# Performance work log

Measured on AMD Instinct MI355X. Metric: run time of the kernel, lower is better.

## Reference

```python
import jax, jax.numpy as jnp
import numpy as np

D_MODEL = 256; N_HEADS = 8; N_LEVELS = 4; N_POINTS = 4; D_FFN = 1024
BS = 8; NQ = 100; NKPT = 17
LEVEL_SHAPES = [(160, 160), (80, 80), (40, 40), (20, 20)]  # (H, W) per level
LEN_V = sum(h * w for h, w in LEVEL_SHAPES)  # 34000


def layer_norm(x, g, b, eps=1e-5):
    m = x.mean(-1, keepdims=True)
    v = ((x - m) ** 2).mean(-1, keepdims=True)
    return (x - m) * jax.lax.rsqrt(v + eps) * g + b


def mha(q, k, v, Wqkv, bqkv, Wo, bo):
    # torch nn.MultiheadAttention, batch_first, eval mode (no dropout)
    d = q.shape[-1]; dh = d // N_HEADS
    def proj(x, W, b):
        return (x @ W.T + b).reshape(*x.shape[:-1], N_HEADS, dh)
    qp = proj(q, Wqkv[:d], bqkv[:d])
    kp = proj(k, Wqkv[d:2 * d], bqkv[d:2 * d])
    vp = proj(v, Wqkv[2 * d:], bqkv[2 * d:])
    att = jnp.einsum('bqhd,bkhd->bhqk', qp, kp) / jnp.sqrt(jnp.asarray(dh, q.dtype))
    att = jax.nn.softmax(att, -1)
    out = jnp.einsum('bhqk,bkhd->bqhd', att, vp).reshape(q.shape)
    return out @ Wo.T + bo


def bilinear_sample(val, loc, h, w):
    # val: (B, H, h*w, Dh); loc: (B, Lq, H, P, 2) normalized to [0,1]
    # matches F.grid_sample(align_corners=False, padding_mode='zeros') on grid 2*loc-1
    B, Lq, H, P, _ = loc.shape
    px = loc[..., 0] * w - 0.5
    py = loc[..., 1] * h - 0.5
    x0f = jnp.floor(px); y0f = jnp.floor(py)
    lx = px - x0f; ly = py - y0f
    x0 = x0f.astype(jnp.int32); y0 = y0f.astype(jnp.int32)
    out = jnp.zeros((B, H, Lq, P, val.shape[-1]), val.dtype)
    for dx, dy, wt in ((0, 0, (1 - lx) * (1 - ly)), (1, 0, lx * (1 - ly)),
                       (0, 1, (1 - lx) * ly), (1, 1, lx * ly)):
        xi = x0 + dx; yi = y0 + dy
        valid = ((xi >= 0) & (xi < w) & (yi >= 0) & (yi < h)).astype(val.dtype)
        idx = jnp.clip(yi, 0, h - 1) * w + jnp.clip(xi, 0, w - 1)  # (B,Lq,H,P)
        idx = idx.transpose(0, 2, 1, 3).reshape(B, H, Lq * P)
        g = jnp.take_along_axis(val, idx[..., None], axis=2).reshape(B, H, Lq, P, -1)
        out = out + g * (wt * valid).transpose(0, 2, 1, 3)[..., None]
    return out  # (B, H, Lq, P, Dh)


def ms_deform_attn(query, ref_points, memory, off_W, off_b, aw_W, aw_b,
                   val_W, val_b, outp_W, outp_b):
    B, Lq, _ = query.shape
    dh = D_MODEL // N_HEADS
    value = (memory @ val_W.T + val_b).reshape(B, LEN_V, N_HEADS, dh)
    off = (query @ off_W.T + off_b).reshape(B, Lq, N_HEADS, N_LEVELS, N_POINTS, 2)
    aw = (query @ aw_W.T + aw_b).reshape(B, Lq, N_HEADS, N_LEVELS * N_POINTS)
    aw = jax.nn.softmax(aw, -1).reshape(B, Lq, N_HEADS, N_LEVELS, N_POINTS)
    normalizer = jnp.array([[w, h] for h, w in LEVEL_SHAPES], dtype=query.dtype)  # (L,2) as (W,H)
    loc = ref_points[:, :, None, :, None, :] + off / normalizer[None, None, None, :, None, :]
    out = jnp.zeros((B, Lq, N_HEADS, dh), query.dtype)
    start = 0
    for l, (h, w) in enumerate(LEVEL_SHAPES):
        vl = value[:, start:start + h * w].transpose(0, 2, 1, 3)  # (B,H,hw,Dh)
        s = bilinear_sample(vl, loc[:, :, :, l], h, w)            # (B,H,Lq,P,Dh)
        out = out + jnp.einsum('bhqpd,bqhp->bqhd', s, aw[:, :, :, l])
        start += h * w
    return out.reshape(B, Lq, D_MODEL) @ outp_W.T + outp_b


def setup_inputs() -> dict:
    key = jax.random.key(0)
    ks = iter(jax.random.split(key, 40))
    d = D_MODEL
    def w(shape, s=0.02):
        return jax.random.normal(next(ks), shape, jnp.float32) * s
    inp = {
        'tgt_pose': jax.random.normal(next(ks), (BS, NQ, NKPT, d), jnp.float32),
        'tgt_pose_query_pos': jax.random.normal(next(ks), (BS, NQ, NKPT, d), jnp.float32),
        'tgt_pose_reference_points': jax.random.uniform(next(ks), (BS, NQ * NKPT, N_LEVELS, 2), jnp.float32),
        'memory': jax.random.normal(next(ks), (BS, LEN_V, d), jnp.float32),
        'win_Wqkv': w((3 * d, d)), 'win_bqkv': jnp.zeros((3 * d,), jnp.float32),
        'win_Wo': w((d, d)), 'win_bo': jnp.zeros((d,), jnp.float32),
        'win_ng': jnp.ones((d,), jnp.float32), 'win_nb': jnp.zeros((d,), jnp.float32),
        'acr_Wqkv': w((3 * d, d)), 'acr_bqkv': jnp.zeros((3 * d,), jnp.float32),
        'acr_Wo': w((d, d)), 'acr_bo': jnp.zeros((d,), jnp.float32),
        'acr_ng': jnp.ones((d,), jnp.float32), 'acr_nb': jnp.zeros((d,), jnp.float32),
        'off_W': w((N_HEADS * N_LEVELS * N_POINTS * 2, d)),
        'off_b': jax.random.uniform(next(ks), (N_HEADS * N_LEVELS * N_POINTS * 2,), jnp.float32, -1.0, 1.0),
        'aw_W': w((N_HEADS * N_LEVELS * N_POINTS, d)), 'aw_b': jnp.zeros((N_HEADS * N_LEVELS * N_POINTS,), jnp.float32),
        'val_W': w((d, d)), 'val_b': jnp.zeros((d,), jnp.float32),
        'outp_W': w((d, d)), 'outp_b': jnp.zeros((d,), jnp.float32),
        'gate_W': w((2 * d, 2 * d)), 'gate_b': jnp.zeros((2 * d,), jnp.float32),
        'gate_ng': jnp.ones((d,), jnp.float32), 'gate_nb': jnp.zeros((d,), jnp.float32),
        'ffn_W1': w((D_FFN, d)), 'ffn_b1': jnp.zeros((D_FFN,), jnp.float32),
        'ffn_W2': w((d, D_FFN)), 'ffn_b2': jnp.zeros((d,), jnp.float32),
        'n2_g': jnp.ones((d,), jnp.float32), 'n2_b': jnp.zeros((d,), jnp.float32),
        'memory_spatial_shapes': jnp.array(LEVEL_SHAPES, jnp.int32),
    }
    return inp


def reference(tgt_pose, tgt_pose_query_pos, tgt_pose_reference_points, memory,
              win_Wqkv, win_bqkv, win_Wo, win_bo, win_ng, win_nb,
              acr_Wqkv, acr_bqkv, acr_Wo, acr_bo, acr_ng, acr_nb,
              off_W, off_b, aw_W, aw_b, val_W, val_b, outp_W, outp_b,
              gate_W, gate_b, gate_ng, gate_nb,
              ffn_W1, ffn_b1, ffn_W2, ffn_b2, n2_g, n2_b,
              memory_spatial_shapes):
    bs, nq, K, d = tgt_pose.shape
    # with_pos_embed mutates tgt_pose in place in the torch code -> residual includes pos
    tgt = tgt_pose + tgt_pose_query_pos
    # within-attention over keypoints of each query
    x = tgt.reshape(bs * nq, K, d)
    t2 = mha(x, x, x, win_Wqkv, win_bqkv, win_Wo, win_bo).reshape(bs, nq, K, d)
    tgt = layer_norm(tgt + t2, win_ng, win_nb)
    # across-attention over queries for each keypoint
    xk = tgt.transpose(0, 2, 1, 3).reshape(bs * K, nq, d)
    t2 = mha(xk, xk, xk, acr_Wqkv, acr_bqkv, acr_Wo, acr_bo)
    tgt = layer_norm(xk + t2, acr_ng, acr_nb).reshape(bs, K, nq, d).transpose(0, 2, 1, 3)
    # second in-place pos add before deformable cross-attn (also feeds gateway)
    tgt_q = tgt + tgt_pose_query_pos
    t2 = ms_deform_attn(tgt_q.reshape(bs, nq * K, d), tgt_pose_reference_points, memory,
                        off_W, off_b, aw_W, aw_b, val_W, val_b, outp_W, outp_b)
    t2 = t2.reshape(bs, nq, K, d)
    # Gate
    g = jax.nn.sigmoid(jnp.concatenate([tgt_q, t2], -1) @ gate_W.T + gate_b)
    g1, g2 = jnp.split(g, 2, -1)
    tgt = layer_norm(g1 * tgt_q + g2 * t2, gate_ng, gate_nb)
    # FFN
    h = jax.nn.relu(tgt @ ffn_W1.T + ffn_b1)
    tgt = tgt + h @ ffn_W2.T + ffn_b2
    tgt = layer_norm(jnp.clip(tgt, -65504.0, 65504.0), n2_g, n2_b)
    return tgt
```

## Files before the change

kernel.cpp:

```cpp
#include <hip/hip_runtime.h>
#include <hip/hip_bf16.h>

#define NH 8
#define BS_ 8
#define NQ_ 100
#define NK_ 17
#define LQ 1700
#define T_TOK 13600
#define LEN_VV 34000

typedef __attribute__((ext_vector_type(8))) short short8v;
typedef __attribute__((ext_vector_type(8))) __bf16 bf16x8;
typedef __attribute__((ext_vector_type(4))) float f32x4;

__device__ __forceinline__ short f2bf(float f){
  __hip_bfloat16 h = __float2bfloat16(f);
  return *reinterpret_cast<short*>(&h);
}
__device__ __forceinline__ float bf2f(short s){
  return __uint_as_float(((uint)(unsigned short)s) << 16);
}

template<int EPI, int ADDA, int SWZ>
__global__ __launch_bounds__(256) void mgemm_k(const float* __restrict__ A,
                                               const float* __restrict__ A2,
                                               const float* __restrict__ W,
                                               const float* __restrict__ bias,
                                               __hip_bfloat16* __restrict__ Cb,
                                               int M, int N, int K, int nbx){
  __shared__ short sh[128 * 136];
  short* As = sh;
  short* Ws = sh + 128 * 64;
  int j;
  if (SWZ){
    int total = gridDim.x;
    int q = total >> 3, r = total & 7;
    int x = blockIdx.x & 7, k = blockIdx.x >> 3;
    j = (x < r) ? x * (q + 1) + k : r * (q + 1) + (x - r) * q + k;
  } else {
    j = blockIdx.x;
  }
  const int tid = threadIdx.x;
  const int bm = (j / nbx) * 128, bn = (j % nbx) * 128;
  const int wave = tid >> 6, lane = tid & 63;
  const int wm = (wave >> 1) * 64, wn = (wave & 1) * 64;
  const int s = tid & 7;
  const int row0 = tid >> 3;
  f32x4 acc[4][4] = {};
  const int lrow = lane & 15, lk = lane >> 4;

  float4 ra[8], rw[8];
#pragma unroll
  for (int i = 0; i < 4; i++){
    int row = row0 + i * 32;
    int gr = bm + row;
    float4 z = make_float4(0.f, 0.f, 0.f, 0.f);
    if (gr < M){
      const float* p = A + (size_t)gr * K + s * 8;
      float4 x0 = ((const float4*)p)[0], x1 = ((const float4*)p)[1];
      if (ADDA){
        const float* q2 = A2 + (size_t)gr * K + s * 8;
        float4 y0 = ((const float4*)q2)[0], y1 = ((const float4*)q2)[1];
        x0.x+=y0.x; x0.y+=y0.y; x0.z+=y0.z; x0.w+=y0.w;
        x1.x+=y1.x; x1.y+=y1.y; x1.z+=y1.z; x1.w+=y1.w;
      }
      ra[2 * i] = x0; ra[2 * i + 1] = x1;
    } else { ra[2 * i] = z; ra[2 * i + 1] = z; }
    const float* q = W + (size_t)(bn + row) * K + s * 8;
    rw[2 * i] = ((const float4*)q)[0]; rw[2 * i + 1] = ((const float4*)q)[1];
  }

  for (int k0 = 0; k0 < K; k0 += 64){
#pragma unroll
    for (int i = 0; i < 4; i++){
      int row = row0 + i * 32;
      int sw = ((s ^ (row & 7)) << 3) + row * 64;
      float4 a0 = ra[2 * i], a1 = ra[2 * i + 1];
      short8v v;
      v[0]=f2bf(a0.x); v[1]=f2bf(a0.y); v[2]=f2bf(a0.z); v[3]=f2bf(a0.w);
      v[4]=f2bf(a1.x); v[5]=f2bf(a1.y); v[6]=f2bf(a1.z); v[7]=f2bf(a1.w);
      *(short8v*)&As[sw] = v;
      a0 = rw[2 * i]; a1 = rw[2 * i + 1];
      short8v u;
      u[0]=f2bf(a0.x); u[1]=f2bf(a0.y); u[2]=f2bf(a0.z); u[3]=f2bf(a0.w);
      u[4]=f2bf(a1.x); u[5]=f2bf(a1.y); u[6]=f2bf(a1.z); u[7]=f2bf(a1.w);
      *(short8v*)&Ws[sw] = u;
    }
    __syncthreads();
    if (k0 + 64 < K){
#pragma unroll
      for (int i = 0; i < 4; i++){
        int row = row0 + i * 32;
        int gr = bm + row;
        float4 z = make_float4(0.f, 0.f, 0.f, 0.f);
        if (gr < M){
          const float* p = A + (size_t)gr * K + k0 + 64 + s * 8;
          float4 x0 = ((const float4*)p)[0], x1 = ((const float4*)p)[1];
          if (ADDA){
            const float* q2 = A2 + (size_t)gr * K + k0 + 64 + s * 8;
            float4 y0 = ((const float4*)q2)[0], y1 = ((const float4*)q2)[1];
            x0.x+=y0.x; x0.y+=y0.y; x0.z+=y0.z; x0.w+=y0.w;
            x1.x+=y1.x; x1.y+=y1.y; x1.z+=y1.z; x1.w+=y1.w;
          }
          ra[2 * i] = x0; ra[2 * i + 1] = x1;
        } else { ra[2 * i] = z; ra[2 * i + 1] = z; }
        const float* q = W + (size_t)(bn + row) * K + k0 + 64 + s * 8;
        rw[2 * i] = ((const float4*)q)[0]; rw[2 * i + 1] = ((const float4*)q)[1];
      }
    }
#pragma unroll
    for (int ks = 0; ks < 2; ks++){
      short8v af[4], bw[4];
      int slot = ks * 4 + lk;
#pragma unroll
      for (int m = 0; m < 4; m++){
        int r = wm + m * 16 + lrow;
        af[m] = *(const short8v*)&As[r * 64 + ((slot ^ (r & 7)) << 3)];
      }
#pragma unroll
      for (int n = 0; n < 4; n++){
        int r = wn + n * 16 + lrow;
        bw[n] = *(const short8v*)&Ws[r * 64 + ((slot ^ (r & 7)) << 3)];
      }
#pragma unroll
      for (int m = 0; m < 4; m++)
#pragma unroll
        for (int n = 0; n < 4; n++)
          acc[m][n] = __builtin_amdgcn_mfma_f32_16x16x32_bf16(
              __builtin_bit_cast(bf16x8, af[m]),
              __builtin_bit_cast(bf16x8, bw[n]), acc[m][n], 0, 0, 0);
    }
    __syncthreads();
  }
  const int STR = 136;
#pragma unroll
  for (int n = 0; n < 4; n++){
    int col = wn + n * 16 + lrow;
    float bsv = bias[bn + col];
#pragma unroll
    for (int m = 0; m < 4; m++){
#pragma unroll
      for (int i = 0; i < 4; i++){
        int row = wm + m * 16 + lk * 4 + i;
        float c = acc[m][n][i] + bsv;
        if (EPI == 1) c = fmaxf(c, 0.f);
        sh[row * STR + col] = f2bf(c);
      }
    }
  }
  __syncthreads();
#pragma unroll
  for (int it = 0; it < 8; it++){
    int r = it * 16 + (tid >> 4);
    int chunk = tid & 15;
    if (bm + r < M){
      uint4 v = *(const uint4*)((const char*)sh + r * 272 + chunk * 16);
      *(uint4*)((char*)Cb + ((size_t)(bm + r) * N + bn) * 2 + chunk * 16) = v;
    }
  }
}

template<int EPI, int OUTB, int INB, int DUALA>
__global__ __launch_bounds__(256) void g64_k(const void* __restrict__ Av,
                                             const void* __restrict__ A1v,
                                             const float* __restrict__ W0,
                                             const float* __restrict__ W1,
                                             int NSPLIT,
                                             const float* __restrict__ bias0,
                                             const float* __restrict__ bias1,
                                             const float* __restrict__ RES,
                                             float* __restrict__ Cf,
                                             __hip_bfloat16* __restrict__ Cb,
                                             int M, int N, int K, int sA){
  __shared__ short sh64[2 * 64 * 64];
  short* As = sh64;
  short* Ws = sh64 + 64 * 64;
  const int tid = threadIdx.x;
  const int bn = blockIdx.x * 64, bm = blockIdx.y * 64;
  const int wave = tid >> 6, lane = tid & 63;
  const int wm = (wave >> 1) * 32, wn = (wave & 1) * 32;
  const int s = tid & 7, row0 = tid >> 3;
  const int lrow = lane & 15, lk = lane >> 4;
  f32x4 acc[2][2] = {};

  for (int k0 = 0; k0 < K; k0 += 64){
#pragma unroll
    for (int i = 0; i < 2; i++){
      int row = row0 + i * 32;
      int sw = ((s ^ (row & 7)) << 3) + row * 64;
      short8v v = {};
      int gr = bm + row;
      if (gr < M){
        if (INB){
          v = *(const short8v*)((const short*)Av + (size_t)gr * sA + k0 + s * 8);
        } else {
          const float* Ap;
          if (DUALA) Ap = (k0 < 256) ? (const float*)Av + (size_t)gr * 256 + k0
                                     : (const float*)A1v + (size_t)gr * 256 + (k0 - 256);
          else Ap = (const float*)Av + (size_t)gr * sA + k0;
          float4 a0 = ((const float4*)(Ap + s * 8))[0];
          float4 a1 = ((const float4*)(Ap + s * 8))[1];
          v[0]=f2bf(a0.x); v[1]=f2bf(a0.y); v[2]=f2bf(a0.z); v[3]=f2bf(a0.w);
          v[4]=f2bf(a1.x); v[5]=f2bf(a1.y); v[6]=f2bf(a1.z); v[7]=f2bf(a1.w);
        }
      }
      *(short8v*)&As[sw] = v;
      int wr = bn + row;
      const float* Wp = (wr < NSPLIT) ? W0 + (size_t)wr * K + k0
                                      : W1 + (size_t)(wr - NSPLIT) * K + k0;
      float4 b0 = ((const float4*)(Wp + s * 8))[0];
      float4 b1 = ((const float4*)(Wp + s * 8))[1];
      short8v u;
      u[0]=f2bf(b0.x); u[1]=f2bf(b0.y); u[2]=f2bf(b0.z); u[3]=f2bf(b0.w);
      u[4]=f2bf(b1.x); u[5]=f2bf(b1.y); u[6]=f2bf(b1.z); u[7]=f2bf(b1.w);
      *(short8v*)&Ws[sw] = u;
    }
    __syncthreads();
#pragma unroll
    for (int ks = 0; ks < 2; ks++){
      int slot = ks * 4 + lk;
      short8v af[2], bw[2];
#pragma unroll
      for (int m = 0; m < 2; m++){
        int r = wm + m * 16 + lrow;
        af[m] = *(const short8v*)&As[r * 64 + ((slot ^ (r & 7)) << 3)];
      }
#pragma unroll
      for (int n = 0; n < 2; n++){
        int r = wn + n * 16 + lrow;
        bw[n] = *(const short8v*)&Ws[r * 64 + ((slot ^ (r & 7)) << 3)];
      }
#pragma unroll
      for (int m = 0; m < 2; m++)
#pragma unroll
        for (int n = 0; n < 2; n++)
          acc[m][n] = __builtin_amdgcn_mfma_f32_16x16x32_bf16(
              __builtin_bit_cast(bf16x8, af[m]),
              __builtin_bit_cast(bf16x8, bw[n]), acc[m][n], 0, 0, 0);
    }
    __syncthreads();
  }
  if (OUTB){
    const int STR = 72;
#pragma unroll
    for (int n = 0; n < 2; n++){
      int col = wn + n * 16 + lrow;
      int gc = bn + col;
      float bsv = (gc < NSPLIT) ? bias0[gc] : bias1[gc - NSPLIT];
#pragma unroll
      for (int m = 0; m < 2; m++){
#pragma unroll
        for (int i = 0; i < 4; i++){
          int row = wm + m * 16 + lk * 4 + i;
          float c = acc[m][n][i] + bsv;
          if (EPI == 1) c = fmaxf(c, 0.f);
          if (EPI == 2) c = 1.f / (1.f + expf(-c));
          sh64[row * STR + col] = f2bf(c);
        }
      }
    }
    __syncthreads();
#pragma unroll
    for (int it = 0; it < 2; it++){
      int r = it * 32 + (tid >> 3);
      int chunk = tid & 7;
      if (bm + r < M){
        uint4 v = *(const uint4*)((const char*)sh64 + r * 144 + chunk * 16);
        *(uint4*)((char*)Cb + ((size_t)(bm + r) * N + bn) * 2 + chunk * 16) = v;
      }
    }
  } else {
#pragma unroll
    for (int n = 0; n < 2; n++){
      int gc = bn + wn + n * 16 + lrow;
      float bsv = (gc < NSPLIT) ? bias0[gc] : bias1[gc - NSPLIT];
#pragma unroll
      for (int m = 0; m < 2; m++){
#pragma unroll
        for (int i = 0; i < 4; i++){
          int row = bm + wm + m * 16 + lk * 4 + i;
          if (row >= M) continue;
          float c = acc[m][n][i] + bsv;
          if (EPI == 1) c = fmaxf(c, 0.f);
          if (EPI == 2) c = 1.f / (1.f + expf(-c));
          if (EPI == 3) c += RES[(size_t)row * N + gc];
          Cf[(size_t)row * N + gc] = c;
        }
      }
    }
  }
}

template<int SITE, int OUTB>
__global__ __launch_bounds__(512) void gln_k(const short* __restrict__ Abf,
                                             const float* __restrict__ W,
                                             const float* __restrict__ bias,
                                             const float* __restrict__ r0,
                                             const float* __restrict__ r1,
                                             const float* __restrict__ g,
                                             const float* __restrict__ be,
                                             void* __restrict__ outv,
                                             int M, int K){
  __shared__ short As[64 * 64];
  __shared__ short Ws[256 * 64];
  __shared__ float part[64][4][2];
  __shared__ float stats[64][2];
  const int tid = threadIdx.x;
  const int bm = blockIdx.x * 64;
  const int wave = tid >> 6, lane = tid & 63;
  const int wm = (wave >> 2) * 32, wn = (wave & 3) * 64;
  const int s = tid & 7, row0 = tid >> 3;
  const int lrow = lane & 15, lk = lane >> 4;
  f32x4 acc[2][4] = {};

  short8v pa = {};
  { int gr = bm + row0; if (gr < M) pa = *(const short8v*)(Abf + (size_t)gr * K + s * 8); }
  float4 pw[8];
#pragma unroll
  for (int i = 0; i < 4; i++){
    const float* wp = W + (size_t)(row0 + i * 64) * K + s * 8;
    pw[2 * i] = ((const float4*)wp)[0]; pw[2 * i + 1] = ((const float4*)wp)[1];
  }

  for (int k0 = 0; k0 < K; k0 += 64){
    *(short8v*)&As[row0 * 64 + ((s ^ (row0 & 7)) << 3)] = pa;
#pragma unroll
    for (int i = 0; i < 4; i++){
      int row = row0 + i * 64;
      float4 b0 = pw[2 * i], b1 = pw[2 * i + 1];
      short8v u;
      u[0]=f2bf(b0.x); u[1]=f2bf(b0.y); u[2]=f2bf(b0.z); u[3]=f2bf(b0.w);
      u[4]=f2bf(b1.x); u[5]=f2bf(b1.y); u[6]=f2bf(b1.z); u[7]=f2bf(b1.w);
      *(short8v*)&Ws[row * 64 + ((s ^ (row & 7)) << 3)] = u;
    }
    __syncthreads();
    if (k0 + 64 < K){
      int gr = bm + row0;
      pa = (short8v){};
      if (gr < M) pa = *(const short8v*)(Abf + (size_t)gr * K + k0 + 64 + s * 8);
#pragma unroll
      for (int i = 0; i < 4; i++){
        const float* wp = W + (size_t)(row0 + i * 64) * K + k0 + 64 + s * 8;
        pw[2 * i] = ((const float4*)wp)[0]; pw[2 * i + 1] = ((const float4*)wp)[1];
      }
    }
#pragma unroll
    for (int ks = 0; ks < 2; ks++){
      int slot = ks * 4 + lk;
      short8v af[2], bw[4];
#pragma unroll
      for (int m = 0; m < 2; m++){
        int r = wm + m * 16 + lrow;
        af[m] = *(const short8v*)&As[r * 64 + ((slot ^ (r & 7)) << 3)];
      }
#pragma unroll
      for (int n = 0; n < 4; n++){
        int r = wn + n * 16 + lrow;
        bw[n] = *(const short8v*)&Ws[r * 64 + ((slot ^ (r & 7)) << 3)];
      }
#pragma unroll
      for (int m = 0; m < 2; m++)
#pragma unroll
        for (int n = 0; n < 4; n++)
          acc[m][n] = __builtin_amdgcn_mfma_f32_16x16x32_bf16(
              __builtin_bit_cast(bf16x8, af[m]),
              __builtin_bit_cast(bf16x8, bw[n]), acc[m][n], 0, 0, 0);
    }
    __syncthreads();
  }

#pragma unroll
  for (int m = 0; m < 2; m++){
#pragma unroll
    for (int i = 0; i < 4; i++){
      int row = wm + m * 16 + lk * 4 + i;
      int grow = bm + row;
      float s1 = 0.f, s2 = 0.f;
      if (grow < M){
#pragma unroll
        for (int n = 0; n < 4; n++){
          int col = wn + n * 16 + lrow;
          float x = acc[m][n][i] + bias[col] + r0[(size_t)grow * 256 + col];
          if (SITE == 0) x += r1[(size_t)grow * 256 + col];
          if (SITE == 2) x = fminf(fmaxf(x, -65504.f), 65504.f);
          acc[m][n][i] = x;
          s1 += x; s2 += x * x;
        }
      }
#pragma unroll
      for (int msk = 1; msk <= 8; msk <<= 1){
        s1 += __shfl_xor(s1, msk, 64);
        s2 += __shfl_xor(s2, msk, 64);
      }
      if (lrow == 0){ part[row][wave & 3][0] = s1; part[row][wave & 3][1] = s2; }
    }
  }
  __syncthreads();
  if (tid < 64){
    float s1 = part[tid][0][0] + part[tid][1][0] + part[tid][2][0] + part[tid][3][0];
    float s2 = part[tid][0][1] + part[tid][1][1] + part[tid][2][1] + part[tid][3][1];
    float mean = s1 * (1.f / 256.f);
    float var = s2 * (1.f / 256.f) - mean * mean;
    stats[tid][0] = mean;
    stats[tid][1] = rsqrtf(fmaxf(var, 0.f) + 1e-5f);
  }
  __syncthreads();
#pragma unroll
  for (int m = 0; m < 2; m++){
#pragma unroll
    for (int i = 0; i < 4; i++){
      int row = wm + m * 16 + lk * 4 + i;
      int grow = bm + row;
      if (grow >= M) continue;
      float mean = stats[row][0], rstd = stats[row][1];
      size_t orow = grow;
      if (SITE == 0){
        int bi = grow / LQ; int rem = grow % LQ; int q = rem / NK_; int kk = rem % NK_;
        orow = (size_t)bi * LQ + kk * NQ_ + q;
      }
      if (SITE == 1){
        int bi = grow / LQ; int rem = grow % LQ; int kk = rem / NQ_; int q = rem % NQ_;
        orow = (size_t)bi * LQ + q * NK_ + kk;
      }
#pragma unroll
      for (int n = 0; n < 4; n++){
        int col = wn + n * 16 + lrow;
        float o = (acc[m][n][i] - mean) * rstd * g[col] + be[col];
        if (SITE == 1) o += r1[orow * 256 + col];
        if (OUTB) ((short*)outv)[orow * 256 + col] = f2bf(o);
        else      ((float*)outv)[orow * 256 + col] = o;
      }
    }
  }
}

__global__ __launch_bounds__(512) void gateln_k(const short* __restrict__ TQ,
                                                const short* __restrict__ T2,
                                                const float* __restrict__ W,
                                                const float* __restrict__ bias,
                                                const float* __restrict__ g,
                                                const float* __restrict__ be,
                                                float* __restrict__ out, int M){
  __shared__ short sh[64 * 64 + 512 * 64];
  short* As = sh;
  short* Ws = sh + 64 * 64;
  const int tid = threadIdx.x;
  const int bm = blockIdx.x * 64;
  const int wave = tid >> 6, lane = tid & 63;
  const int wm = (wave >> 2) * 32, wn = (wave & 3) * 128;
  const int s = tid & 7, row0 = tid >> 3;
  const int lrow = lane & 15, lk = lane >> 4;
  f32x4 acc[2][8] = {};

  for (int k0 = 0; k0 < 512; k0 += 64){
    {
      short8v v = {};
      int gr = bm + row0;
      if (gr < M){
        v = (k0 < 256) ? *(const short8v*)(TQ + (size_t)gr * 256 + k0 + s * 8)
                       : *(const short8v*)(T2 + (size_t)gr * 256 + (k0 - 256) + s * 8);
      }
      *(short8v*)&As[row0 * 64 + ((s ^ (row0 & 7)) << 3)] = v;
    }
#pragma unroll
    for (int i = 0; i < 8; i++){
      int row = row0 + i * 64;
      const float* wp = W + (size_t)row * 512 + k0 + s * 8;
      float4 b0 = ((const float4*)wp)[0], b1 = ((const float4*)wp)[1];
      short8v u;
      u[0]=f2bf(b0.x); u[1]=f2bf(b0.y); u[2]=f2bf(b0.z); u[3]=f2bf(b0.w);
      u[4]=f2bf(b1.x); u[5]=f2bf(b1.y); u[6]=f2bf(b1.z); u[7]=f2bf(b1.w);
      *(short8v*)&Ws[row * 64 + ((s ^ (row & 7)) << 3)] = u;
    }
    __syncthreads();
#pragma unroll
    for (int ks = 0; ks < 2; ks++){
      int slot = ks * 4 + lk;
      short8v af[2], bw[8];
#pragma unroll
      for (int m = 0; m < 2; m++){
        int r = wm + m * 16 + lrow;
        af[m] = *(const short8v*)&As[r * 64 + ((slot ^ (r & 7)) << 3)];
      }
#pragma unroll
      for (int n = 0; n < 8; n++){
        int r = wn + n * 16 + lrow;
        bw[n] = *(const short8v*)&Ws[r * 64 + ((slot ^ (r & 7)) << 3)];
      }
#pragma unroll
      for (int m = 0; m < 2; m++)
#pragma unroll
        for (int n = 0; n < 8; n++)
          acc[m][n] = __builtin_amdgcn_mfma_f32_16x16x32_bf16(
              __builtin_bit_cast(bf16x8, af[m]),
              __builtin_bit_cast(bf16x8, bw[n]), acc[m][n], 0, 0, 0);
    }
    __syncthreads();
  }
  short* gb = sh;
  const int GSTR = 520;
#pragma unroll
  for (int n = 0; n < 8; n++){
    int col = wn + n * 16 + lrow;
    float bsv = bias[col];
#pragma unroll
    for (int m = 0; m < 2; m++){
#pragma unroll
      for (int i = 0; i < 4; i++){
        int row = wm + m * 16 + lk * 4 + i;
        float c = acc[m][n][i] + bsv;
        gb[row * GSTR + col] = f2bf(1.f / (1.f + __expf(-c)));
      }
    }
  }
  __syncthreads();
  {
    int row = tid >> 3, cg = tid & 7;
    int grow = bm + row;
    float x[32];
    float s1 = 0.f, s2 = 0.f;
    if (grow < M){
#pragma unroll
      for (int jv = 0; jv < 4; jv++){
        int c0 = cg * 32 + jv * 8;
        short8v aqv = *(const short8v*)(TQ + (size_t)grow * 256 + c0);
        short8v t2v = *(const short8v*)(T2 + (size_t)grow * 256 + c0);
#pragma unroll
        for (int jj = 0; jj < 8; jj++){
          float g1 = bf2f(gb[row * GSTR + c0 + jj]);
          float g2 = bf2f(gb[row * GSTR + 256 + c0 + jj]);
          float xv = g1 * bf2f(aqv[jj]) + g2 * bf2f(t2v[jj]);
          x[jv * 8 + jj] = xv; s1 += xv; s2 += xv * xv;
        }
      }
    }
    s1 += __shfl_xor(s1, 1, 64); s2 += __shfl_xor(s2, 1, 64);
    s1 += __shfl_xor(s1, 2, 64); s2 += __shfl_xor(s2, 2, 64);
    s1 += __shfl_xor(s1, 4, 64); s2 += __shfl_xor(s2, 4, 64);
    float mean = s1 * (1.f / 256.f);
    float var = s2 * (1.f / 256.f) - mean * mean;
    float rstd = rsqrtf(fmaxf(var, 0.f) + 1e-5f);
    if (grow < M){
#pragma unroll
      for (int jv = 0; jv < 4; jv++){
        int c0 = cg * 32 + jv * 8;
        float4 o0, o1;
        float* po = (float*)&o0;
#pragma unroll
        for (int jj = 0; jj < 8; jj++){
          int c = c0 + jj;
          float o = (x[jv * 8 + jj] - mean) * rstd * g[c] + be[c];
          if (jj < 4) ((float*)&o0)[jj] = o; else ((float*)&o1)[jj - 4] = o;
        }
        (void)po;
        *(float4*)(out + (size_t)grow * 256 + c0) = o0;
        *(float4*)(out + (size_t)grow * 256 + c0 + 4) = o1;
      }
    }
  }
}

template<int TP, int NSPL>
__global__ __launch_bounds__(256) void mha_mfma_k(const short* __restrict__ qkv,
                                                  __hip_bfloat16* __restrict__ out, int S){
  constexpr int MT = TP / 16;
  constexpr int KSTEPS = (TP + 31) / 32;
  constexpr int KS32 = KSTEPS * 32;
  constexpr int VSTRB = (KS32 == 128) ? 256 : 128;
  constexpr int CH = (MT + NSPL - 1) / NSPL;
  __shared__ short QK[2][TP][64];
  __shared__ short Vt[2][32][VSTRB / 2];
  __shared__ float Sc[2][16][128];
  __shared__ float rinv[2][16];

  const int tid = threadIdx.x;
  const int bid = blockIdx.x;
  const int batch = bid / (4 * NSPL);
  const int rem = bid % (4 * NSPL);
  const int hp = rem / NSPL;
  const int half = rem % NSPL;
  const int mtlo = half * CH;
  const int mthi = (mtlo + CH < MT) ? (mtlo + CH) : MT;
  const int wave = tid >> 6, lane = tid & 63;
  const int hh = wave >> 1, wsub = wave & 1;
  const int lrow = lane & 15, lk = lane >> 4;
  const float scale = 0.17677669529663687f;
  const size_t qbase = (size_t)batch * S * 768;

  for (int idx = tid; idx < 2 * TP * 4; idx += 256){
    int h2 = idx >= TP * 4;
    int rm = idx - h2 * TP * 4;
    int j = rm >> 2, s = rm & 3;
    int h = hp * 2 + h2;
    short8v qv = {}, kv = {};
    if (j < S){
      const short* p = qkv + qbase + (size_t)j * 768 + h * 32 + s * 8;
      qv = *(const short8v*)p;
      kv = *(const short8v*)(p + 256);
    }
    *(short8v*)&QK[h2][j][(s ^ (j & 7)) << 3] = qv;
    *(short8v*)&QK[h2][j][((s + 4) ^ (j & 7)) << 3] = kv;
  }
  for (int idx = tid; idx < 2 * KS32 * 4; idx += 256){
    int h2 = idx >= KS32 * 4;
    int rm = idx - h2 * KS32 * 4;
    int j = rm >> 2, e8 = rm & 3;
    int h = hp * 2 + h2;
    short8v v = {};
    if (j < S) v = *(const short8v*)(qkv + qbase + (size_t)j * 768 + h * 32 + 512 + e8 * 8);
#pragma unroll
    for (int c = 0; c < 8; c++){
      int e = e8 * 8 + c;
      char* pb = (char*)&Vt[h2][0][0] + e * VSTRB + (((j >> 3) ^ (e & 7)) << 4) + ((j & 7) << 1);
      *(short*)pb = v[c];
    }
  }
  __syncthreads();

  for (int mt = mtlo; mt < mthi; mt++){
    for (int nt = wsub; nt < MT; nt += 2){
      int ar = mt * 16 + lrow;
      short8v aq = *(const short8v*)&QK[hh][ar][(lk ^ (ar & 7)) << 3];
      int br = nt * 16 + lrow;
      short8v bk = *(const short8v*)&QK[hh][br][((lk + 4) ^ (br & 7)) << 3];
      f32x4 z = {};
      f32x4 d = __builtin_amdgcn_mfma_f32_16x16x32_bf16(
          __builtin_bit_cast(bf16x8, aq), __builtin_bit_cast(bf16x8, bk), z, 0, 0, 0);
#pragma unroll
      for (int i = 0; i < 4; i++){
        int rr = lk * 4 + i;
        int c = nt * 16 + lrow;
        Sc[hh][rr][(((c >> 2) ^ (rr & 7)) << 2) + (c & 3)] = d[i] * scale;
      }
    }
    __syncthreads();
    if (wsub == 0){
      int rr = lane >> 2, p = lane & 3;
      int grow = mt * 16 + rr;
      int Seff = (grow < S) ? S : 0;
      float mx = -1e30f;
#pragma unroll
      for (int m = 0; m < KSTEPS; m++){
        int j = p + 4 * m;
#pragma unroll
        for (int hf = 0; hf < 2; hf++){
          int ls = 2 * j + hf;
          float4 v = *(const float4*)&Sc[hh][rr][(ls ^ (rr & 7)) << 2];
          int c0 = ls * 4;
          mx = fmaxf(mx, (c0 + 0 < Seff) ? v.x : -1e30f);
          mx = fmaxf(mx, (c0 + 1 < Seff) ? v.y : -1e30f);
          mx = fmaxf(mx, (c0 + 2 < Seff) ? v.z : -1e30f);
          mx = fmaxf(mx, (c0 + 3 < Seff) ? v.w : -1e30f);
        }
      }
      mx = fmaxf(mx, __shfl_xor(mx, 1, 64));
      mx = fmaxf(mx, __shfl_xor(mx, 2, 64));
      float sum = 0.f;
#pragma unroll
      for (int m = 0; m < KSTEPS; m++){
        int j = p + 4 * m;
        float ev[8];
#pragma unroll
        for (int hf = 0; hf < 2; hf++){
          int ls = 2 * j + hf;
          float4 v = *(const float4*)&Sc[hh][rr][(ls ^ (rr & 7)) << 2];
          int c0 = ls * 4;
          ev[hf * 4 + 0] = (c0 + 0 < Seff) ? __expf(v.x - mx) : 0.f;
          ev[hf * 4 + 1] = (c0 + 1 < Seff) ? __expf(v.y - mx) : 0.f;
          ev[hf * 4 + 2] = (c0 + 2 < Seff) ? __expf(v.z - mx) : 0.f;
          ev[hf * 4 + 3] = (c0 + 3 < Seff) ? __expf(v.w - mx) : 0.f;
        }
        short8v pb;
#pragma unroll
        for (int q2 = 0; q2 < 8; q2++){ pb[q2] = f2bf(ev[q2]); sum += ev[q2]; }
        *(short8v*)((char*)&Sc[hh][rr][0] + ((j ^ (rr & 7)) << 4)) = pb;
      }
      sum += __shfl_xor(sum, 1, 64);
      sum += __shfl_xor(sum, 2, 64);
      if (p == 0) rinv[hh][rr] = (sum > 0.f) ? 1.f / sum : 0.f;
    }
    __syncthreads();
    {
      int nt2 = wsub;
      f32x4 acc = {};
#pragma unroll
      for (int ks = 0; ks < KSTEPS; ks++){
        int slot = ks * 4 + lk;
        short8v ap = *(const short8v*)((const char*)&Sc[hh][lrow][0] + ((slot ^ (lrow & 7)) << 4));
        int e = nt2 * 16 + lrow;
        short8v bv = *(const short8v*)((const char*)&Vt[hh][0][0] + e * VSTRB + ((slot ^ (e & 7)) << 4));
        acc = __builtin_amdgcn_mfma_f32_16x16x32_bf16(
            __builtin_bit_cast(bf16x8, ap), __builtin_bit_cast(bf16x8, bv), acc, 0, 0, 0);
      }
      int h = hp * 2 + hh;
#pragma unroll
      for (int i = 0; i < 4; i++){
        int row = mt * 16 + lk * 4 + i;
        if (row < S){
          float rv = rinv[hh][lk * 4 + i];
          out[((size_t)batch * S + row) * 256 + h * 32 + nt2 * 16 + lrow] =
              __float2bfloat16(acc[i] * rv);
        }
      }
    }
    __syncthreads();
  }
}

__global__ __launch_bounds__(256) void deform_k(const __hip_bfloat16* __restrict__ val,
                                                const float* __restrict__ offaw,
                                                const float* __restrict__ ref,
                                                unsigned int* __restrict__ outb){
  __shared__ uint2 meta[32][16][4];
  const int tid = threadIdx.x;
  const int t0 = blockIdx.x * 4;
  {
    int g = tid >> 3;
    int pair = tid & 7;
    int lt = g >> 3, h = g & 7;
    int t = t0 + lt;
    int b = t / LQ;
    int p0 = pair * 2;
    int l = p0 >> 2;
    const int starts[4] = {0, 25600, 32000, 33600};
    const int HS[4] = {160, 80, 40, 20};
    int w = HS[l];
    const float* ap = offaw + (size_t)t * 384 + 256 + h * 16;
    float a0 = ap[p0];
    float a1 = ap[p0 + 1];
    float mx = fmaxf(a0, a1);
#pragma unroll
    for (int m = 1; m <= 4; m <<= 1) mx = fmaxf(mx, __shfl_xor(mx, m, 64));
    float e0 = expf(a0 - mx), e1 = expf(a1 - mx);
    float s = e0 + e1;
#pragma unroll
    for (int m = 1; m <= 4; m <<= 1) s += __shfl_xor(s, m, 64);
    float inv = 1.f / s;
    float rx = ref[((size_t)t * 4 + l) * 2 + 0];
    float ry = ref[((size_t)t * 4 + l) * 2 + 1];
    float4 ov = *(const float4*)(offaw + (size_t)t * 384 + h * 32 + l * 8 + p0 * 2);
    int vbase = (b * LEN_VV + starts[l]) * 128 + h * 16;
#pragma unroll
    for (int pp = 0; pp < 2; pp++){
      float wgt = (pp ? e1 : e0) * inv;
      float px = rx * w + (pp ? ov.z : ov.x) - 0.5f;
      float py = ry * w + (pp ? ov.w : ov.y) - 0.5f;
      float x0f = floorf(px), y0f = floorf(py);
      float lx = px - x0f, ly = py - y0f;
      int x0 = (int)x0f, y0 = (int)y0f;
#pragma unroll
      for (int c = 0; c < 4; c++){
        int dx = c & 1, dy = c >> 1;
        int xi = x0 + dx, yi = y0 + dy;
        bool ok = (xi >= 0) & (xi < w) & (yi >= 0) & (yi < w);
        float cw = ok ? wgt * (dx ? lx : 1.f - lx) * (dy ? ly : 1.f - ly) : 0.f;
        uint idx = ok ? (uint)(vbase + (yi * w + xi) * 128) : 0u;
        uint2 m2; m2.x = idx; m2.y = __float_as_uint(cw);
        meta[g][p0 + pp][c] = m2;
      }
    }
  }
  __syncthreads();
  const uint2* V2 = (const uint2*)val;
  int sg = tid >> 3, lane8 = tid & 7;
  int lt = sg >> 3, h = sg & 7;
  int t = t0 + lt;
  float a0 = 0.f, a1 = 0.f, a2 = 0.f, a3 = 0.f;
#pragma unroll 4
  for (int c = 0; c < 64; c++){
    uint2 mw = meta[sg][c >> 2][c & 3];
    float wv = __uint_as_float(mw.y);
    uint2 v = V2[(size_t)(mw.x >> 1) + lane8];
    a0 += wv * __uint_as_float(v.x << 16);
    a1 += wv * __uint_as_float(v.x & 0xffff0000u);
    a2 += wv * __uint_as_float(v.y << 16);
    a3 += wv * __uint_as_float(v.y & 0xffff0000u);
  }
  uint2 u;
  u.x = ((uint)(unsigned short)f2bf(a1) << 16) | (uint)(unsigned short)f2bf(a0);
  u.y = ((uint)(unsigned short)f2bf(a3) << 16) | (uint)(unsigned short)f2bf(a2);
  ((uint2*)outb)[((size_t)t * 256 + h * 32) / 4 + lane8] = u;
}

extern "C" void kernel_launch(void* const* d_in, const int* in_sizes, int n_in,
                              void* d_out, int out_size, void* d_ws, size_t ws_size,
                              hipStream_t stream){
  const float* tgt_pose = (const float*)d_in[0];
  const float* qpos     = (const float*)d_in[1];
  const float* refp     = (const float*)d_in[2];
  const float* memory   = (const float*)d_in[3];
  const float* win_Wqkv = (const float*)d_in[4];
  const float* win_bqkv = (const float*)d_in[5];
  const float* win_Wo   = (const float*)d_in[6];
  const float* win_bo   = (const float*)d_in[7];
  const float* win_ng   = (const float*)d_in[8];
  const float* win_nb   = (const float*)d_in[9];
  const float* acr_Wqkv = (const float*)d_in[10];
  const float* acr_bqkv = (const float*)d_in[11];
  const float* acr_Wo   = (const float*)d_in[12];
  const float* acr_bo   = (const float*)d_in[13];
  const float* acr_ng   = (const float*)d_in[14];
  const float* acr_nb   = (const float*)d_in[15];
  const float* off_W    = (const float*)d_in[16];
  const float* off_b    = (const float*)d_in[17];
  const float* aw_W     = (const float*)d_in[18];
  const float* aw_b     = (const float*)d_in[19];
  const float* val_W    = (const float*)d_in[20];
  const float* val_b    = (const float*)d_in[21];
  const float* outp_W   = (const float*)d_in[22];
  const float* outp_b   = (const float*)d_in[23];
  const float* gate_W   = (const float*)d_in[24];
  const float* gate_b   = (const float*)d_in[25];
  const float* gate_ng  = (const float*)d_in[26];
  const float* gate_nb  = (const float*)d_in[27];
  const float* ffn_W1   = (const float*)d_in[28];
  const float* ffn_b1   = (const float*)d_in[29];
  const float* ffn_W2   = (const float*)d_in[30];
  const float* ffn_b2   = (const float*)d_in[31];
  const float* n2_g     = (const float*)d_in[32];
  const float* n2_b     = (const float*)d_in[33];

  float* out = (float*)d_out;
  char* ws = (char*)d_ws;
  const size_t TB = (size_t)T_TOK * 256 * 4;
  float* B1 = (float*)(ws);
  float* B2 = (float*)(ws + TB);
  char* p = ws + 2 * TB;
  short* Qb  = (short*)p;  p += (size_t)T_TOK * 768 * 2;
  short* ABF = (short*)p;  p += (size_t)T_TOK * 256 * 2;
  short* TQb = (short*)p;  p += (size_t)T_TOK * 256 * 2;
  short* T2b = (short*)p;  p += (size_t)T_TOK * 256 * 2;
  float* OFFAW = (float*)p; p += (size_t)T_TOK * 384 * 4;
  char* Vregion = p;
  __hip_bfloat16* V = (__hip_bfloat16*)Vregion;
  short* FF = (short*)Vregion;

  const int GM128 = (T_TOK + 127) / 128;
  const int GM64  = (T_TOK + 63) / 64;
  const int BIG = 1 << 30;

  mgemm_k<0,0,1><<<2 * 2125, 256, 0, stream>>>(memory, nullptr, val_W, val_b, V, BS_ * LEN_VV, 256, 256, 2);
  mgemm_k<0,1,0><<<6 * GM128, 256, 0, stream>>>(tgt_pose, qpos, win_Wqkv, win_bqkv, (__hip_bfloat16*)Qb, T_TOK, 768, 256, 6);
  mha_mfma_k<32,1><<<800 * 4, 256, 0, stream>>>(Qb, (__hip_bfloat16*)ABF, 17);
  gln_k<0,0><<<GM64, 512, 0, stream>>>(ABF, win_Wo, win_bo, tgt_pose, qpos, win_ng, win_nb, B1, T_TOK, 256);
  mgemm_k<0,0,0><<<6 * GM128, 256, 0, stream>>>(B1, nullptr, acr_Wqkv, acr_bqkv, (__hip_bfloat16*)Qb, T_TOK, 768, 256, 6);
  mha_mfma_k<112,2><<<136 * 8, 256, 0, stream>>>(Qb, (__hip_bfloat16*)ABF, 100);
  gln_k<1,1><<<GM64, 512, 0, stream>>>(ABF, acr_Wo, acr_bo, B1, qpos, acr_ng, acr_nb, TQb, T_TOK, 256);
  g64_k<0,0,1,0><<<dim3(6, GM64), 256, 0, stream>>>(TQb, nullptr, off_W, aw_W, 256, off_b, aw_b, nullptr, OFFAW, nullptr, T_TOK, 384, 256, 256);
  deform_k<<<T_TOK / 4, 256, 0, stream>>>(V, OFFAW, refp, (unsigned int*)ABF);
  g64_k<0,1,1,0><<<dim3(4, GM64), 256, 0, stream>>>(ABF, nullptr, outp_W, outp_W, BIG, outp_b, outp_b, nullptr, nullptr, (__hip_bfloat16*)T2b, T_TOK, 256, 256, 256);
  gateln_k<<<GM64, 512, 0, stream>>>(TQb, T2b, gate_W, gate_b, gate_ng, gate_nb, B2, T_TOK);
  mgemm_k<1,0,0><<<8 * GM128, 256, 0, stream>>>(B2, nullptr, ffn_W1, ffn_b1, (__hip_bfloat16*)FF, T_TOK, 1024, 256, 8);
  gln_k<2,0><<<GM64, 512, 0, stream>>>(FF, ffn_W2, ffn_b2, B2, nullptr, n2_g, n2_b, out, T_TOK, 1024);
}
```

Measured before the change: 462.3 us.

## Fuse across-attn out-proj LayerNorm with offset/weight GEMM; store intermediate in bf16

Adds a kernel that computes the across-attention output projection, residual add and LayerNorm, adds the query position, and then runs the sampling-offset and attention-weight GEMM on the normalized tile held in shared memory. This removes one kernel launch and the global round trip of the TQ activations before the offset GEMM. The within-attention LayerNorm output is now stored as bf16 instead of fp32, and the QKV GEMM gains a bf16-input path, which halves that buffer's traffic and skips a conversion. In exchange the fused kernel has one block per 64 rows and reloads all 384 weight rows with a synchronisation at each K step, with no prefetch, so it may lose some parallelism and overlap.

```diff
diff --git a/kernel.cpp b/kernel.cpp
--- a/kernel.cpp
+++ b/kernel.cpp
@@ -21,8 +21,8 @@
   return __uint_as_float(((uint)(unsigned short)s) << 16);
 }
 
-template<int EPI, int ADDA, int SWZ>
-__global__ __launch_bounds__(256) void mgemm_k(const float* __restrict__ A,
+template<int EPI, int ADDA, int SWZ, int INB>
+__global__ __launch_bounds__(256) void mgemm_k(const void* __restrict__ Av,
                                                const float* __restrict__ A2,
                                                const float* __restrict__ W,
                                                const float* __restrict__ bias,
@@ -40,6 +40,8 @@
   } else {
     j = blockIdx.x;
   }
+  const float* A = (const float*)Av;
+  const short* Ab = (const short*)Av;
   const int tid = threadIdx.x;
   const int bm = (j / nbx) * 128, bn = (j % nbx) * 128;
   const int wave = tid >> 6, lane = tid & 63;
@@ -49,23 +51,29 @@
   f32x4 acc[4][4] = {};
   const int lrow = lane & 15, lk = lane >> 4;
 
-  float4 ra[8], rw[8];
+  float4 ra[INB ? 1 : 8], rw[8];
+  short8v rab[INB ? 4 : 1];
 #pragma unroll
   for (int i = 0; i < 4; i++){
     int row = row0 + i * 32;
     int gr = bm + row;
-    float4 z = make_float4(0.f, 0.f, 0.f, 0.f);
-    if (gr < M){
-      const float* p = A + (size_t)gr * K + s * 8;
-      float4 x0 = ((const float4*)p)[0], x1 = ((const float4*)p)[1];
-      if (ADDA){
-        const float* q2 = A2 + (size_t)gr * K + s * 8;
-        float4 y0 = ((const float4*)q2)[0], y1 = ((const float4*)q2)[1];
-        x0.x+=y0.x; x0.y+=y0.y; x0.z+=y0.z; x0.w+=y0.w;
-        x1.x+=y1.x; x1.y+=y1.y; x1.z+=y1.z; x1.w+=y1.w;
-      }
-      ra[2 * i] = x0; ra[2 * i + 1] = x1;
-    } else { ra[2 * i] = z; ra[2 * i + 1] = z; }
+    if (INB){
+      short8v z = {};
+      rab[INB ? i : 0] = (gr < M) ? *(const short8v*)(Ab + (size_t)gr * K + s * 8) : z;
+    } else {
+      float4 z = make_float4(0.f, 0.f, 0.f, 0.f);
+      if (gr < M){
+        const float* p = A + (size_t)gr * K + s * 8;
+        float4 x0 = ((const float4*)p)[0], x1 = ((const float4*)p)[1];
+        if (ADDA){
+          const float* q2 = A2 + (size_t)gr * K + s * 8;
+          float4 y0 = ((const float4*)q2)[0], y1 = ((const float4*)q2)[1];
+          x0.x+=y0.x; x0.y+=y0.y; x0.z+=y0.z; x0.w+=y0.w;
+          x1.x+=y1.x; x1.y+=y1.y; x1.z+=y1.z; x1.w+=y1.w;
+        }
+        ra[INB ? 0 : (2 * i)] = x0; ra[INB ? 0 : (2 * i + 1)] = x1;
+      } else { ra[INB ? 0 : (2 * i)] = z; ra[INB ? 0 : (2 * i + 1)] = z; }
+    }
     const float* q = W + (size_t)(bn + row) * K + s * 8;
     rw[2 * i] = ((const float4*)q)[0]; rw[2 * i + 1] = ((const float4*)q)[1];
   }
@@ -75,12 +83,16 @@
     for (int i = 0; i < 4; i++){
       int row = row0 + i * 32;
       int sw = ((s ^ (row & 7)) << 3) + row * 64;
-      float4 a0 = ra[2 * i], a1 = ra[2 * i + 1];
-      short8v v;
-      v[0]=f2bf(a0.x); v[1]=f2bf(a0.y); v[2]=f2bf(a0.z); v[3]=f2bf(a0.w);
-      v[4]=f2bf(a1.x); v[5]=f2bf(a1.y); v[6]=f2bf(a1.z); v[7]=f2bf(a1.w);
-      *(short8v*)&As[sw] = v;
-      a0 = rw[2 * i]; a1 = rw[2 * i + 1];
+      if (INB){
+        *(short8v*)&As[sw] = rab[INB ? i : 0];
+      } else {
+        float4 a0 = ra[INB ? 0 : (2 * i)], a1 = ra[INB ? 0 : (2 * i + 1)];
+        short8v v;
+        v[0]=f2bf(a0.x); v[1]=f2bf(a0.y); v[2]=f2bf(a0.z); v[3]=f2bf(a0.w);
+        v[4]=f2bf(a1.x); v[5]=f2bf(a1.y); v[6]=f2bf(a1.z); v[7]=f2bf(a1.w);
+        *(short8v*)&As[sw] = v;
+      }
+      float4 a0 = rw[2 * i], a1 = rw[2 * i + 1];
       short8v u;
       u[0]=f2bf(a0.x); u[1]=f2bf(a0.y); u[2]=f2bf(a0.z); u[3]=f2bf(a0.w);
       u[4]=f2bf(a1.x); u[5]=f2bf(a1.y); u[6]=f2bf(a1.z); u[7]=f2bf(a1.w);
@@ -92,18 +104,23 @@
       for (int i = 0; i < 4; i++){
         int row = row0 + i * 32;
         int gr = bm + row;
-        float4 z = make_float4(0.f, 0.f, 0.f, 0.f);
-        if (gr < M){
-          const float* p = A + (size_t)gr * K + k0 + 64 + s * 8;
-          float4 x0 = ((const float4*)p)[0], x1 = ((const float4*)p)[1];
-          if (ADDA){
-            const float* q2 = A2 + (size_t)gr * K + k0 + 64 + s * 8;
-            float4 y0 = ((const float4*)q2)[0], y1 = ((const float4*)q2)[1];
-            x0.x+=y0.x; x0.y+=y0.y; x0.z+=y0.z; x0.w+=y0.w;
-            x1.x+=y1.x; x1.y+=y1.y; x1.z+=y1.z; x1.w+=y1.w;
-          }
-          ra[2 * i] = x0; ra[2 * i + 1] = x1;
-        } else { ra[2 * i] = z; ra[2 * i + 1] = z; }
+        if (INB){
+          short8v z = {};
+          rab[INB ? i : 0] = (gr < M) ? *(const short8v*)(Ab + (size_t)gr * K + k0 + 64 + s * 8) : z;
+        } else {
+          float4 z = make_float4(0.f, 0.f, 0.f, 0.f);
+          if (gr < M){
+            const float* p = A + (size_t)gr * K + k0 + 64 + s * 8;
+            float4 x0 = ((const float4*)p)[0], x1 = ((const float4*)p)[1];
+            if (ADDA){
+              const float* q2 = A2 + (size_t)gr * K + k0 + 64 + s * 8;
+              float4 y0 = ((const float4*)q2)[0], y1 = ((const float4*)q2)[1];
+              x0.x+=y0.x; x0.y+=y0.y; x0.z+=y0.z; x0.w+=y0.w;
+              x1.x+=y1.x; x1.y+=y1.y; x1.z+=y1.z; x1.w+=y1.w;
+            }
+            ra[INB ? 0 : (2 * i)] = x0; ra[INB ? 0 : (2 * i + 1)] = x1;
+          } else { ra[INB ? 0 : (2 * i)] = z; ra[INB ? 0 : (2 * i + 1)] = z; }
+        }
         const float* q = W + (size_t)(bn + row) * K + k0 + 64 + s * 8;
         rw[2 * i] = ((const float4*)q)[0]; rw[2 * i + 1] = ((const float4*)q)[1];
       }
@@ -418,17 +435,216 @@
         int bi = grow / LQ; int rem = grow % LQ; int q = rem / NK_; int kk = rem % NK_;
         orow = (size_t)bi * LQ + kk * NQ_ + q;
       }
-      if (SITE == 1){
-        int bi = grow / LQ; int rem = grow % LQ; int kk = rem / NQ_; int q = rem % NQ_;
-        orow = (size_t)bi * LQ + q * NK_ + kk;
-      }
 #pragma unroll
       for (int n = 0; n < 4; n++){
         int col = wn + n * 16 + lrow;
         float o = (acc[m][n][i] - mean) * rstd * g[col] + be[col];
-        if (SITE == 1) o += r1[orow * 256 + col];
         if (OUTB) ((short*)outv)[orow * 256 + col] = f2bf(o);
         else      ((float*)outv)[orow * 256 + col] = o;
+      }
+    }
+  }
+}
+
+__global__ __launch_bounds__(512) void glnoa_k(const short* __restrict__ Abf,
+                                               const float* __restrict__ W,
+                                               const float* __restrict__ bias,
+                                               const short* __restrict__ r0b,
+                                               const float* __restrict__ qpos,
+                                               const float* __restrict__ g,
+                                               const float* __restrict__ be,
+                                               short* __restrict__ TQout,
+                                               float* __restrict__ OFFAW,
+                                               const float* __restrict__ off_W,
+                                               const float* __restrict__ aw_W,
+                                               const float* __restrict__ off_b,
+                                               const float* __restrict__ aw_b,
+                                               int M){
+  __shared__ short smem[64 * 256 + 384 * 64];
+  short* As1 = smem;
+  short* Ws1 = smem + 64 * 64;
+  float* part = (float*)(smem + 64 * 64 + 256 * 64);
+  float* stats = part + 64 * 4 * 2;
+  short* As2 = smem;
+  short* Ws2 = smem + 64 * 256;
+  const int K = 256;
+  const int tid = threadIdx.x;
+  const int bm = blockIdx.x * 64;
+  const int wave = tid >> 6, lane = tid & 63;
+  const int wm = (wave >> 2) * 32, wn = (wave & 3) * 64;
+  const int s = tid & 7, row0 = tid >> 3;
+  const int lrow = lane & 15, lk = lane >> 4;
+  f32x4 acc[2][4] = {};
+
+  short8v pa = {};
+  { int gr = bm + row0; if (gr < M) pa = *(const short8v*)(Abf + (size_t)gr * K + s * 8); }
+  float4 pw[8];
+#pragma unroll
+  for (int i = 0; i < 4; i++){
+    const float* wp = W + (size_t)(row0 + i * 64) * K + s * 8;
+    pw[2 * i] = ((const float4*)wp)[0]; pw[2 * i + 1] = ((const float4*)wp)[1];
+  }
+  for (int k0 = 0; k0 < K; k0 += 64){
+    *(short8v*)&As1[row0 * 64 + ((s ^ (row0 & 7)) << 3)] = pa;
+#pragma unroll
+    for (int i = 0; i < 4; i++){
+      int row = row0 + i * 64;
+      float4 b0 = pw[2 * i], b1 = pw[2 * i + 1];
+      short8v u;
+      u[0]=f2bf(b0.x); u[1]=f2bf(b0.y); u[2]=f2bf(b0.z); u[3]=f2bf(b0.w);
+      u[4]=f2bf(b1.x); u[5]=f2bf(b1.y); u[6]=f2bf(b1.z); u[7]=f2bf(b1.w);
+      *(short8v*)&Ws1[row * 64 + ((s ^ (row & 7)) << 3)] = u;
+    }
+    __syncthreads();
+    if (k0 + 64 < K){
+      int gr = bm + row0;
+      pa = (short8v){};
+      if (gr < M) pa = *(const short8v*)(Abf + (size_t)gr * K + k0 + 64 + s * 8);
+#pragma unroll
+      for (int i = 0; i < 4; i++){
+        const float* wp = W + (size_t)(row0 + i * 64) * K + k0 + 64 + s * 8;
+        pw[2 * i] = ((const float4*)wp)[0]; pw[2 * i + 1] = ((const float4*)wp)[1];
+      }
+    }
+#pragma unroll
+    for (int ks = 0; ks < 2; ks++){
+      int slot = ks * 4 + lk;
+      short8v af[2], bw[4];
+#pragma unroll
+      for (int m = 0; m < 2; m++){
+        int r = wm + m * 16 + lrow;
+        af[m] = *(const short8v*)&As1[r * 64 + ((slot ^ (r & 7)) << 3)];
+      }
+#pragma unroll
+      for (int n = 0; n < 4; n++){
+        int r = wn + n * 16 + lrow;
+        bw[n] = *(const short8v*)&Ws1[r * 64 + ((slot ^ (r & 7)) << 3)];
+      }
+#pragma unroll
+      for (int m = 0; m < 2; m++)
+#pragma unroll
+        for (int n = 0; n < 4; n++)
+          acc[m][n] = __builtin_amdgcn_mfma_f32_16x16x32_bf16(
+              __builtin_bit_cast(bf16x8, af[m]),
+              __builtin_bit_cast(bf16x8, bw[n]), acc[m][n], 0, 0, 0);
+    }
+    __syncthreads();
+  }
+#pragma unroll
+  for (int m = 0; m < 2; m++){
+#pragma unroll
+    for (int i = 0; i < 4; i++){
+      int row = wm + m * 16 + lk * 4 + i;
+      int grow = bm + row;
+      float s1 = 0.f, s2 = 0.f;
+      if (grow < M){
+#pragma unroll
+        for (int n = 0; n < 4; n++){
+          int col = wn + n * 16 + lrow;
+          float x = acc[m][n][i] + bias[col] + bf2f(r0b[(size_t)grow * 256 + col]);
+          acc[m][n][i] = x;
+          s1 += x; s2 += x * x;
+        }
+      }
+#pragma unroll
+      for (int msk = 1; msk <= 8; msk <<= 1){
+        s1 += __shfl_xor(s1, msk, 64);
+        s2 += __shfl_xor(s2, msk, 64);
+      }
+      if (lrow == 0){ part[(row * 4 + (wave & 3)) * 2] = s1; part[(row * 4 + (wave & 3)) * 2 + 1] = s2; }
+    }
+  }
+  __syncthreads();
+  if (tid < 64){
+    float s1 = part[(tid * 4 + 0) * 2] + part[(tid * 4 + 1) * 2] + part[(tid * 4 + 2) * 2] + part[(tid * 4 + 3) * 2];
+    float s2 = part[(tid * 4 + 0) * 2 + 1] + part[(tid * 4 + 1) * 2 + 1] + part[(tid * 4 + 2) * 2 + 1] + part[(tid * 4 + 3) * 2 + 1];
+    float mean = s1 * (1.f / 256.f);
+    float var = s2 * (1.f / 256.f) - mean * mean;
+    stats[tid * 2] = mean;
+    stats[tid * 2 + 1] = rsqrtf(fmaxf(var, 0.f) + 1e-5f);
+  }
+  __syncthreads();
+#pragma unroll
+  for (int m = 0; m < 2; m++){
+#pragma unroll
+    for (int i = 0; i < 4; i++){
+      int row = wm + m * 16 + lk * 4 + i;
+      int grow = bm + row;
+      float mean = stats[row * 2], rstd = stats[row * 2 + 1];
+      size_t orow = 0;
+      if (grow < M){
+        int bi = grow / LQ; int rem = grow % LQ; int kk = rem / NQ_; int q = rem % NQ_;
+        orow = (size_t)bi * LQ + q * NK_ + kk;
+      }
+#pragma unroll
+      for (int n = 0; n < 4; n++){
+        int col = wn + n * 16 + lrow;
+        float tq = 0.f;
+        if (grow < M){
+          float o = (acc[m][n][i] - mean) * rstd * g[col] + be[col];
+          tq = o + qpos[orow * 256 + col];
+          TQout[orow * 256 + col] = f2bf(tq);
+        }
+        As2[row * 256 + ((((col >> 3) ^ (row & 7)) << 3) + (col & 7))] = f2bf(tq);
+      }
+    }
+  }
+  __syncthreads();
+  const int wm2 = (wave >> 2) * 32, wn2 = (wave & 3) * 96;
+  f32x4 acc2[2][6] = {};
+  for (int k0 = 0; k0 < 256; k0 += 64){
+#pragma unroll
+    for (int it = 0; it < 6; it++){
+      int wr = row0 + it * 64;
+      const float* Wp = (wr < 256) ? off_W + (size_t)wr * 256 + k0
+                                   : aw_W + (size_t)(wr - 256) * 256 + k0;
+      float4 b0 = ((const float4*)(Wp + s * 8))[0];
+      float4 b1 = ((const float4*)(Wp + s * 8))[1];
+      short8v u;
+      u[0]=f2bf(b0.x); u[1]=f2bf(b0.y); u[2]=f2bf(b0.z); u[3]=f2bf(b0.w);
+      u[4]=f2bf(b1.x); u[5]=f2bf(b1.y); u[6]=f2bf(b1.z); u[7]=f2bf(b1.w);
+      *(short8v*)&Ws2[wr * 64 + ((s ^ (wr & 7)) << 3)] = u;
+    }
+    __syncthreads();
+#pragma unroll
+    for (int ks = 0; ks < 2; ks++){
+      int slotl = ks * 4 + lk;
+      int slotg = (k0 >> 3) + slotl;
+      short8v af[2], bw[6];
+#pragma unroll
+      for (int m = 0; m < 2; m++){
+        int r = wm2 + m * 16 + lrow;
+        af[m] = *(const short8v*)&As2[r * 256 + ((slotg ^ (r & 7)) << 3)];
+      }
+#pragma unroll
+      for (int n = 0; n < 6; n++){
+        int r = wn2 + n * 16 + lrow;
+        bw[n] = *(const short8v*)&Ws2[r * 64 + ((slotl ^ (r & 7)) << 3)];
+      }
+#pragma unroll
+      for (int m = 0; m < 2; m++)
+#pragma unroll
+        for (int n = 0; n < 6; n++)
+          acc2[m][n] = __builtin_amdgcn_mfma_f32_16x16x32_bf16(
+              __builtin_bit_cast(bf16x8, af[m]),
+              __builtin_bit_cast(bf16x8, bw[n]), acc2[m][n], 0, 0, 0);
+    }
+    __syncthreads();
+  }
+#pragma unroll
+  for (int m = 0; m < 2; m++){
+#pragma unroll
+    for (int i = 0; i < 4; i++){
+      int row = wm2 + m * 16 + lk * 4 + i;
+      int grow = bm + row;
+      if (grow >= M) continue;
+      int bi = grow / LQ; int rem = grow % LQ; int kk = rem / NQ_; int q = rem % NQ_;
+      size_t orow = (size_t)bi * LQ + q * NK_ + kk;
+#pragma unroll
+      for (int n = 0; n < 6; n++){
+        int col = wn2 + n * 16 + lrow;
+        float c = acc2[m][n][i] + ((col < 256) ? off_b[col] : aw_b[col - 256]);
+        OFFAW[orow * 384 + col] = c;
       }
     }
   }
@@ -545,14 +761,12 @@
       for (int jv = 0; jv < 4; jv++){
         int c0 = cg * 32 + jv * 8;
         float4 o0, o1;
-        float* po = (float*)&o0;
 #pragma unroll
         for (int jj = 0; jj < 8; jj++){
           int c = c0 + jj;
           float o = (x[jv * 8 + jj] - mean) * rstd * g[c] + be[c];
           if (jj < 4) ((float*)&o0)[jj] = o; else ((float*)&o1)[jj - 4] = o;
         }
-        (void)po;
         *(float4*)(out + (size_t)grow * 256 + c0) = o0;
         *(float4*)(out + (size_t)grow * 256 + c0 + 4) = o1;
       }
@@ -823,9 +1037,9 @@
   float* out = (float*)d_out;
   char* ws = (char*)d_ws;
   const size_t TB = (size_t)T_TOK * 256 * 4;
-  float* B1 = (float*)(ws);
-  float* B2 = (float*)(ws + TB);
-  char* p = ws + 2 * TB;
+  float* B2 = (float*)(ws);
+  char* p = ws + TB;
+  short* B1b = (short*)p;  p += (size_t)T_TOK * 256 * 2;
   short* Qb  = (short*)p;  p += (size_t)T_TOK * 768 * 2;
   short* ABF = (short*)p;  p += (size_t)T_TOK * 256 * 2;
   short* TQb = (short*)p;  p += (size_t)T_TOK * 256 * 2;
@@ -839,17 +1053,17 @@
   const int GM64  = (T_TOK + 63) / 64;
   const int BIG = 1 << 30;
 
-  mgemm_k<0,0,1><<<2 * 2125, 256, 0, stream>>>(memory, nullptr, val_W, val_b, V, BS_ * LEN_VV, 256, 256, 2);
-  mgemm_k<0,1,0><<<6 * GM128, 256, 0, stream>>>(tgt_pose, qpos, win_Wqkv, win_bqkv, (__hip_bfloat16*)Qb, T_TOK, 768, 256, 6);
+  mgemm_k<0,0,1,0><<<2 * 2125, 256, 0, stream>>>(memory, nullptr, val_W, val_b, V, BS_ * LEN_VV, 256, 256, 2);
+  mgemm_k<0,1,0,0><<<6 * GM128, 256, 0, stream>>>(tgt_pose, qpos, win_Wqkv, win_bqkv, (__hip_bfloat16*)Qb, T_TOK, 768, 256, 6);
   mha_mfma_k<32,1><<<800 * 4, 256, 0, stream>>>(Qb, (__hip_bfloat16*)ABF, 17);
-  gln_k<0,0><<<GM64, 512, 0, stream>>>(ABF, win_Wo, win_bo, tgt_pose, qpos, win_ng, win_nb, B1, T_TOK, 256);
-  mgemm_k<0,0,0><<<6 * GM128, 256, 0, stream>>>(B1, nullptr, acr_Wqkv, acr_bqkv, (__hip_bfloat16*)Qb, T_TOK, 768, 256, 6);
+  gln_k<0,1><<<GM64, 512, 0, stream>>>(ABF, win_Wo, win_bo, tgt_pose, qpos, win_ng, win_nb, B1b, T_TOK, 256);
+  mgemm_k<0,0,0,1><<<6 * GM128, 256, 0, stream>>>(B1b, nullptr, acr_Wqkv, acr_bqkv, (__hip_bfloat16*)Qb, T_TOK, 768, 256, 6);
   mha_mfma_k<112,2><<<136 * 8, 256, 0, stream>>>(Qb, (__hip_bfloat16*)ABF, 100);
-  gln_k<1,1><<<GM64, 512, 0, stream>>>(ABF, acr_Wo, acr_bo, B1, qpos, acr_ng, acr_nb, TQb, T_TOK, 256);
-  g64_k<0,0,1,0><<<dim3(6, GM64), 256, 0, stream>>>(TQb, nullptr, off_W, aw_W, 256, off_b, aw_b, nullptr, OFFAW, nullptr, T_TOK, 384, 256, 256);
+  glnoa_k<<<GM64, 512, 0, stream>>>(ABF, acr_Wo, acr_bo, B1b, qpos, acr_ng, acr_nb,
+                                    TQb, OFFAW, off_W, aw_W, off_b, aw_b, T_TOK);
   deform_k<<<T_TOK / 4, 256, 0, stream>>>(V, OFFAW, refp, (unsigned int*)ABF);
   g64_k<0,1,1,0><<<dim3(4, GM64), 256, 0, stream>>>(ABF, nullptr, outp_W, outp_W, BIG, outp_b, outp_b, nullptr, nullptr, (__hip_bfloat16*)T2b, T_TOK, 256, 256, 256);
   gateln_k<<<GM64, 512, 0, stream>>>(TQb, T2b, gate_W, gate_b, gate_ng, gate_nb, B2, T_TOK);
-  mgemm_k<1,0,0><<<8 * GM128, 256, 0, stream>>>(B2, nullptr, ffn_W1, ffn_b1, (__hip_bfloat16*)FF, T_TOK, 1024, 256, 8);
+  mgemm_k<1,0,0,0><<<8 * GM128, 256, 0, stream>>>(B2, nullptr, ffn_W1, ffn_b1, (__hip_bfloat16*)FF, T_TOK, 1024, 256, 8);
   gln_k<2,0><<<GM64, 512, 0, stream>>>(FF, ffn_W2, ffn_b2, B2, nullptr, n2_g, n2_b, out, T_TOK, 1024);
 }
```

Result: no change. 463.7 us (+0.3%).
